# Performance work log

Measured on AMD Instinct MI355X. Metric: run time of the kernel, lower is better.

## Reference

```python
import jax, jax.numpy as jnp
import numpy as np

NUM_RBF = 16
MAX_REL = 32          # max_relative_feature
AUTOREGRESSIVE = True
D_MIN, D_MAX = 2.0, 22.0
LN_EPS = 1e-5


def setup_inputs() -> dict:
    key = jax.random.key(0)
    ks = jax.random.split(key, 6)
    B, L, A, K = 1, 1280, 14, 30
    E_feat, edge_in = 128, 16 + NUM_RBF * 4 * 10  # 656
    X = jax.random.normal(ks[0], (B, L, A, 3), dtype=jnp.float32) * 3.0
    residue_idx = jnp.tile(jnp.arange(L, dtype=jnp.int32)[None], (B, 1))
    chain_labels = jnp.zeros((B, L), dtype=jnp.int32)
    E_idx = jax.random.randint(ks[1], (B, L, K), 0, L, dtype=jnp.int32)
    atom_mask = jnp.ones((B, L, A), dtype=jnp.float32)
    W_pos = jax.random.normal(ks[2], (2 * MAX_REL + 2, 16), dtype=jnp.float32) * 0.1
    b_pos = jnp.zeros((16,), dtype=jnp.float32)
    W_edge = jax.random.normal(ks[3], (edge_in, E_feat), dtype=jnp.float32) * 0.05
    ln_gamma = jnp.ones((E_feat,), dtype=jnp.float32)
    ln_beta = jnp.zeros((E_feat,), dtype=jnp.float32)
    return {"X": X, "residue_idx": residue_idx, "chain_labels": chain_labels,
            "E_idx": E_idx, "atom_mask": atom_mask, "W_pos": W_pos,
            "b_pos": b_pos, "W_edge": W_edge, "ln_gamma": ln_gamma,
            "ln_beta": ln_beta}


def _forward(X, residue_idx, chain_labels, E_idx, W_pos, b_pos, W_edge,
             ln_gamma, ln_beta):
    B, L, A, _ = X.shape
    K = E_idx.shape[-1]
    # backbone atoms in loop order [Ca, N, C, O] -> X indices [1, 0, 2, 3]
    bb = X[:, :, jnp.array([1, 0, 2, 3]), :]          # [B, L, 4, 3]
    sc = X[:, :, 4:, :]                               # [B, L, 10, 3]
    Abb = jnp.transpose(bb, (0, 2, 1, 3))             # [B, 4, L, 3]
    Asc = jnp.transpose(sc, (0, 2, 1, 3))             # [B, 10, L, 3]
    # dense pairwise distances for all 40 (bb, sc) atom pairs: [B,4,10,L,L]
    diff = Abb[:, :, None, :, None, :] - Asc[:, None, :, None, :, :]
    D = jnp.sqrt(jnp.sum(diff * diff, axis=-1) + 1e-6)
    # gather top-k neighbor columns -> [B,4,10,L,K]
    D_nb = jnp.take_along_axis(D, E_idx[:, None, None, :, :], axis=4)
    mu = jnp.linspace(D_MIN, D_MAX, NUM_RBF, dtype=D_nb.dtype)
    sigma = (D_MAX - D_MIN) / NUM_RBF
    RBF = jnp.exp(-(((D_nb[..., None] - mu) / sigma) ** 2))  # [B,4,10,L,K,16]
    if AUTOREGRESSIVE:
        self_edges = (E_idx == jnp.arange(L, dtype=E_idx.dtype)[None, :, None])
        RBF = jnp.where(self_edges[:, None, None, :, :, None], 0.0, RBF)
    # concat order: bb outer, sc inner -> [B,L,K, 4*10*16]
    RBF_all = jnp.transpose(RBF, (0, 3, 4, 1, 2, 5)).reshape(B, L, K, 4 * 10 * NUM_RBF)
    # positional encodings
    offset = residue_idx[:, :, None] - residue_idx[:, None, :]        # [B,L,L]
    offset = jnp.take_along_axis(offset, E_idx, axis=2)               # [B,L,K]
    d_chains = (chain_labels[:, :, None] == chain_labels[:, None, :]).astype(jnp.int32)
    E_chains = jnp.take_along_axis(d_chains, E_idx, axis=2)           # [B,L,K]
    d = jnp.clip(offset + MAX_REL, 0, 2 * MAX_REL) * E_chains + (1 - E_chains) * (2 * MAX_REL + 1)
    d_onehot = jax.nn.one_hot(d, 2 * MAX_REL + 2, dtype=W_pos.dtype)  # [B,L,K,66]
    E_positional = d_onehot @ W_pos + b_pos                           # [B,L,K,16]
    E = jnp.concatenate([E_positional, RBF_all], axis=-1)             # [B,L,K,656]
    E = E @ W_edge                                                    # no bias
    # LayerNorm over last dim
    mean = jnp.mean(E, axis=-1, keepdims=True)
    var = jnp.mean((E - mean) ** 2, axis=-1, keepdims=True)
    E = (E - mean) / jnp.sqrt(var + LN_EPS) * ln_gamma + ln_beta
    return E


def reference(X, residue_idx, chain_labels, E_idx, atom_mask, W_pos, b_pos,
              W_edge, ln_gamma, ln_beta):
    E = _forward(X, residue_idx, chain_labels, E_idx, W_pos, b_pos, W_edge,
                 ln_gamma, ln_beta)
    return (E, E_idx)
```

## Files before the change

kernel.cpp:

```cpp
#include <hip/hip_runtime.h>

typedef short bf16x8 __attribute__((ext_vector_type(8)));
typedef float f32x4  __attribute__((ext_vector_type(4)));

#define L_RES 1280
#define A_ATM 14
#define K_NB  30
#define FEAT  656
#define NKB   21
#define NCH   128
#define FRAG  512
#define E_OUT_OFF (L_RES * K_NB * NCH)
#define NEDGE (L_RES * K_NB)

__device__ __forceinline__ ushort f2bf(float x) {
    union { float f; unsigned u; } v; v.f = x;
    unsigned r = (v.u + 0x7fffu + ((v.u >> 16) & 1u)) >> 16;
    return (ushort)r;
}

__global__ __launch_bounds__(256) void prep_kernel(const float* __restrict__ W,
                                                   ushort* __restrict__ Wpack) {
    int u = blockIdx.x * 256 + threadIdx.x;
    if (u >= 84 * 128) return;
    int kbq = u >> 7, n = u & 127;
    int kb = kbq >> 2, quad = kbq & 3;
    ushort val[8];
#pragma unroll
    for (int j = 0; j < 8; j++) {
        int k = kb * 32 + quad * 8 + j;
        val[j] = (k < FEAT) ? f2bf(W[k * NCH + n]) : (ushort)0;
    }
    ushort* dst = Wpack + (size_t)((((n >> 4) * NKB + kb) * 64 + quad * 16 + (n & 15)) * 8);
    *(ulonglong2*)dst = *(const ulonglong2*)val;
}

__global__ __launch_bounds__(256) void sidechain_fused_kernel(
    const float* __restrict__ X,
    const int*   __restrict__ ridx,
    const int*   __restrict__ clab,
    const int*   __restrict__ Eidx,
    const float* __restrict__ Wpos,
    const float* __restrict__ bpos,
    const ushort* __restrict__ Wpack,
    const float* __restrict__ gamma,
    const float* __restrict__ beta,
    float* __restrict__ out)
{
    __shared__ float scj[4][K_NB][10][3];
    __shared__ float bbs[4][4][3];

    const int t    = threadIdx.x;
    const int w    = t >> 6;
    const int lane = t & 63;
    const int i    = blockIdx.x * 4 + w;
    const int frow = lane & 15;
    const int quad = lane >> 4;

    if (lane < 12) {
        const int perm[4] = {1, 0, 2, 3};
        int a = lane / 3, c = lane - a * 3;
        bbs[w][a][c] = X[(i * A_ATM + perm[a]) * 3 + c];
    }
    for (int idx = lane; idx < K_NB * 30; idx += 64) {
        int e = idx / 30, r = idx - e * 30;
        int a = r / 3, c = r - a * 3;
        int j = Eidx[i * K_NB + e];
        scj[w][e][a][c] = X[(j * A_ATM + 4 + a) * 3 + c];
    }
    if (lane < K_NB) out[E_OUT_OFF + i * K_NB + lane] = (float)Eidx[i * K_NB + lane];

    const int e0 = frow;
    const int e1 = 16 + frow;
    const bool v1 = (e1 < K_NB);
    const int j0 = Eidx[i * K_NB + e0];
    const int j1 = v1 ? Eidx[i * K_NB + e1] : 0;
    const bool rbf0 = (j0 != i);
    const bool rbf1 = v1 && (j1 != i);

    const int ri = ridx[i], ci = clab[i];
    int d0, d1;
    {
        int off0 = ri - ridx[j0] + 32;
        off0 = off0 < 0 ? 0 : (off0 > 64 ? 64 : off0);
        d0 = (ci == clab[j0]) ? off0 : 65;
        int off1 = ri - ridx[j1] + 32;
        off1 = off1 < 0 ? 0 : (off1 > 64 ? 64 : off1);
        d1 = (ci == clab[j1]) ? off1 : 65;
    }

    const ushort* Bbase = Wpack + (size_t)lane * 8;
    f32x4 acc0[8], acc1[8];
#pragma unroll
    for (int n = 0; n < 8; n++) {
        acc0[n] = (f32x4){0.f, 0.f, 0.f, 0.f};
        acc1[n] = (f32x4){0.f, 0.f, 0.f, 0.f};
    }

#pragma unroll
    for (int kb = 0; kb < NKB; kb++) {
        bf16x8 b[8];
#pragma unroll
        for (int n = 0; n < 8; n++)
            b[n] = *(const bf16x8*)(Bbase + (size_t)(n * NKB + kb) * FRAG);

        ushort u0[8], u1[8];
        if (kb == 0 && quad < 2) {
#pragma unroll
            for (int j = 0; j < 8; j++) {
                int c = quad * 8 + j;
                float bp = bpos[c];
                u0[j] = f2bf(Wpos[d0 * 16 + c] + bp);
                u1[j] = v1 ? f2bf(Wpos[d1 * 16 + c] + bp) : (ushort)0;
            }
        } else {
            bool kv = !(kb == NKB - 1 && quad >= 2);
            int p  = kv ? (2 * kb - 1 + (quad >> 1)) : 0;
            int r0 = (quad & 1) * 8;
            int ab = p / 10, as = p - ab * 10;
            float bx = bbs[w][ab][0], by = bbs[w][ab][1], bz = bbs[w][ab][2];
            float x0 = scj[w][e0][as][0], y0 = scj[w][e0][as][1], z0 = scj[w][e0][as][2];
            int e1c = v1 ? e1 : 0;
            float x1 = scj[w][e1c][as][0], y1 = scj[w][e1c][as][1], z1 = scj[w][e1c][as][2];
            float dx0 = bx - x0, dy0 = by - y0, dz0 = bz - z0;
            float dx1 = bx - x1, dy1 = by - y1, dz1 = bz - z1;
            float dist0 = sqrtf(dx0 * dx0 + dy0 * dy0 + dz0 * dz0 + 1e-6f);
            float dist1 = sqrtf(dx1 * dx1 + dy1 * dy1 + dz1 * dz1 + 1e-6f);
            bool m0ok = kv && rbf0, m1ok = kv && rbf1;
#pragma unroll
            for (int j = 0; j < 8; j++) {
                float mu = 2.0f + (float)(r0 + j) * (20.0f / 15.0f);
                float t0 = (dist0 - mu) * 0.8f;
                float t1 = (dist1 - mu) * 0.8f;
                u0[j] = m0ok ? f2bf(__expf(-t0 * t0)) : (ushort)0;
                u1[j] = m1ok ? f2bf(__expf(-t1 * t1)) : (ushort)0;
            }
        }
        bf16x8 a0 = *(const bf16x8*)u0;
        bf16x8 a1 = *(const bf16x8*)u1;
#pragma unroll
        for (int n = 0; n < 8; n++)
            acc0[n] = __builtin_amdgcn_mfma_f32_16x16x32_bf16(a0, b[n], acc0[n], 0, 0, 0);
#pragma unroll
        for (int n = 0; n < 8; n++)
            acc1[n] = __builtin_amdgcn_mfma_f32_16x16x32_bf16(a1, b[n], acc1[n], 0, 0, 0);
    }

    float g[8], bt[8];
#pragma unroll
    for (int n = 0; n < 8; n++) {
        g[n]  = gamma[n * 16 + frow];
        bt[n] = beta[n * 16 + frow];
    }

#pragma unroll
    for (int m = 0; m < 2; m++) {
        f32x4* acc = m ? acc1 : acc0;
#pragma unroll
        for (int r = 0; r < 4; r++) {
            float s = 0.f, q = 0.f;
#pragma unroll
            for (int n = 0; n < 8; n++) {
                float v = acc[n][r];
                s += v; q += v * v;
            }
#pragma unroll
            for (int off = 1; off < 16; off <<= 1) {
                s += __shfl_xor(s, off);
                q += __shfl_xor(q, off);
            }
            float mean = s * (1.0f / 128.0f);
            float var  = q * (1.0f / 128.0f) - mean * mean;
            float rstd = rsqrtf(var + 1e-5f);
            int edge = m * 16 + quad * 4 + r;
            if (edge < K_NB) {
                float* o = out + ((size_t)i * K_NB + edge) * NCH + frow;
#pragma unroll
                for (int n = 0; n < 8; n++)
                    o[n * 16] = (acc[n][r] - mean) * rstd * g[n] + bt[n];
            }
        }
    }
}

extern "C" void kernel_launch(void* const* d_in, const int* in_sizes, int n_in,
                              void* d_out, int out_size, void* d_ws, size_t ws_size,
                              hipStream_t stream) {
    const float* X     = (const float*)d_in[0];
    const int*   ridx  = (const int*)  d_in[1];
    const int*   clab  = (const int*)  d_in[2];
    const int*   Eidx  = (const int*)  d_in[3];
    const float* Wpos  = (const float*)d_in[5];
    const float* bpos  = (const float*)d_in[6];
    const float* Wedge = (const float*)d_in[7];
    const float* gamma = (const float*)d_in[8];
    const float* beta  = (const float*)d_in[9];
    float* out = (float*)d_out;

    ushort* Wpack = (ushort*)d_ws;

    prep_kernel<<<42, 256, 0, stream>>>(Wedge, Wpack);
    sidechain_fused_kernel<<<L_RES / 4, 256, 0, stream>>>(
        X, ridx, clab, Eidx, Wpos, bpos, Wpack, gamma, beta, out);
}
```

Before: 112.5 us.

## Split K dimension across wave pairs with LDS reduction, exp2-based RBF

Each block now handles 2 residues instead of 4. Two waves per residue split the 21 K-blocks of the GEMM and combine their partial accumulators through shared memory before the LayerNorm. This doubles the grid to 640 blocks, which should fill more CUs and halve the serial MFMA chain per wave, at the cost of an extra LDS exchange and a block barrier. The RBF is also rewritten to use exp2 with prescaled constants, and bf16 packing now truncates instead of rounding to nearest even, which slightly changes numerics.

```diff
diff --git a/kernel.cpp b/kernel.cpp
--- a/kernel.cpp
+++ b/kernel.cpp
@@ -1,7 +1,8 @@
 #include <hip/hip_runtime.h>
 
-typedef short bf16x8 __attribute__((ext_vector_type(8)));
-typedef float f32x4  __attribute__((ext_vector_type(4)));
+typedef short    bf16x8 __attribute__((ext_vector_type(8)));
+typedef float    f32x4  __attribute__((ext_vector_type(4)));
+typedef unsigned u32x4  __attribute__((ext_vector_type(4)));
 
 #define L_RES 1280
 #define A_ATM 14
@@ -11,12 +12,15 @@
 #define NCH   128
 #define FRAG  512
 #define E_OUT_OFF (L_RES * K_NB * NCH)
-#define NEDGE (L_RES * K_NB)
 
 __device__ __forceinline__ ushort f2bf(float x) {
     union { float f; unsigned u; } v; v.f = x;
     unsigned r = (v.u + 0x7fffu + ((v.u >> 16) & 1u)) >> 16;
     return (ushort)r;
+}
+__device__ __forceinline__ unsigned pkbf(float lo, float hi) {
+    union { float f; unsigned u; } a, b; a.f = lo; b.f = hi;
+    return (a.u >> 16) | (b.u & 0xffff0000u);
 }
 
 __global__ __launch_bounds__(256) void prep_kernel(const float* __restrict__ W,
@@ -47,49 +51,53 @@
     const float* __restrict__ beta,
     float* __restrict__ out)
 {
-    __shared__ float scj[4][K_NB][10][3];
-    __shared__ float bbs[4][4][3];
-
+    __shared__ __align__(16) float scj[2][K_NB][10][4];
+    __shared__ float bbs[2][4][3];
+    __shared__ __align__(16) float xch[2][16][64][4];
+
+    const int blk  = blockIdx.x;
     const int t    = threadIdx.x;
     const int w    = t >> 6;
     const int lane = t & 63;
-    const int i    = blockIdx.x * 4 + w;
+    const int rh   = w & 1;
+    const int kh   = w >> 1;
+    const int i    = blk * 2 + rh;
     const int frow = lane & 15;
     const int quad = lane >> 4;
 
-    if (lane < 12) {
+    if (t < 24) {
         const int perm[4] = {1, 0, 2, 3};
-        int a = lane / 3, c = lane - a * 3;
-        bbs[w][a][c] = X[(i * A_ATM + perm[a]) * 3 + c];
-    }
-    for (int idx = lane; idx < K_NB * 30; idx += 64) {
-        int e = idx / 30, r = idx - e * 30;
-        int a = r / 3, c = r - a * 3;
-        int j = Eidx[i * K_NB + e];
-        scj[w][e][a][c] = X[(j * A_ATM + 4 + a) * 3 + c];
-    }
-    if (lane < K_NB) out[E_OUT_OFF + i * K_NB + lane] = (float)Eidx[i * K_NB + lane];
-
-    const int e0 = frow;
-    const int e1 = 16 + frow;
+        int r = t / 12, rr = t - r * 12, a = rr / 3, c = rr - a * 3;
+        bbs[r][a][c] = X[((blk * 2 + r) * A_ATM + perm[a]) * 3 + c];
+    }
+#pragma unroll
+    for (int idx = t; idx < 600; idx += 256) {
+        int r = idx / 300, rem = idx - r * 300;
+        int e = rem / 10, a = rem - e * 10;
+        int j = Eidx[(blk * 2 + r) * K_NB + e];
+        const float* xp = X + ((size_t)j * A_ATM + 4 + a) * 3;
+        float4 v = make_float4(xp[0], xp[1], xp[2], 0.f);
+        *(float4*)&scj[r][e][a][0] = v;
+    }
+    __syncthreads();
+
+    const int e0 = frow, e1 = 16 + frow;
     const bool v1 = (e1 < K_NB);
     const int j0 = Eidx[i * K_NB + e0];
     const int j1 = v1 ? Eidx[i * K_NB + e1] : 0;
-    const bool rbf0 = (j0 != i);
-    const bool rbf1 = v1 && (j1 != i);
-
-    const int ri = ridx[i], ci = clab[i];
-    int d0, d1;
+    const bool ok0 = (j0 != i);
+    const bool ok1 = v1 && (j1 != i);
+    int d0 = 65, d1 = 65;
     {
-        int off0 = ri - ridx[j0] + 32;
-        off0 = off0 < 0 ? 0 : (off0 > 64 ? 64 : off0);
-        d0 = (ci == clab[j0]) ? off0 : 65;
-        int off1 = ri - ridx[j1] + 32;
-        off1 = off1 < 0 ? 0 : (off1 > 64 ? 64 : off1);
-        d1 = (ci == clab[j1]) ? off1 : 65;
-    }
-
+        int ci = clab[i], ri = ridx[i];
+        if (ci == clab[j0]) { int o = ri - ridx[j0] + 32; d0 = o < 0 ? 0 : (o > 64 ? 64 : o); }
+        if (ci == clab[j1]) { int o = ri - ridx[j1] + 32; d1 = o < 0 ? 0 : (o > 64 ? 64 : o); }
+    }
+
+    const int kb_lo = kh ? 11 : 0;
+    const int kb_hi = kh ? NKB : 11;
     const ushort* Bbase = Wpack + (size_t)lane * 8;
+
     f32x4 acc0[8], acc1[8];
 #pragma unroll
     for (int n = 0; n < 8; n++) {
@@ -97,87 +105,111 @@
         acc1[n] = (f32x4){0.f, 0.f, 0.f, 0.f};
     }
 
-#pragma unroll
-    for (int kb = 0; kb < NKB; kb++) {
+    const float cs = 0.96089795f;
+    const float mustep = 1.33333333f * cs;
+    const int   r0 = (quad & 1) * 8;
+    const float mubase = (2.0f + (float)r0 * 1.33333333f) * cs;
+
+    for (int kb = kb_lo; kb < kb_hi; kb++) {
         bf16x8 b[8];
 #pragma unroll
         for (int n = 0; n < 8; n++)
             b[n] = *(const bf16x8*)(Bbase + (size_t)(n * NKB + kb) * FRAG);
 
-        ushort u0[8], u1[8];
+        union { u32x4 u; bf16x8 h; } A0, A1;
         if (kb == 0 && quad < 2) {
+            float p0[8], p1[8];
 #pragma unroll
             for (int j = 0; j < 8; j++) {
                 int c = quad * 8 + j;
                 float bp = bpos[c];
-                u0[j] = f2bf(Wpos[d0 * 16 + c] + bp);
-                u1[j] = v1 ? f2bf(Wpos[d1 * 16 + c] + bp) : (ushort)0;
+                p0[j] = Wpos[d0 * 16 + c] + bp;
+                p1[j] = v1 ? (Wpos[d1 * 16 + c] + bp) : 0.f;
+            }
+#pragma unroll
+            for (int jj = 0; jj < 4; jj++) {
+                A0.u[jj] = pkbf(p0[2 * jj], p0[2 * jj + 1]);
+                A1.u[jj] = pkbf(p1[2 * jj], p1[2 * jj + 1]);
             }
         } else {
             bool kv = !(kb == NKB - 1 && quad >= 2);
             int p  = kv ? (2 * kb - 1 + (quad >> 1)) : 0;
-            int r0 = (quad & 1) * 8;
             int ab = p / 10, as = p - ab * 10;
-            float bx = bbs[w][ab][0], by = bbs[w][ab][1], bz = bbs[w][ab][2];
-            float x0 = scj[w][e0][as][0], y0 = scj[w][e0][as][1], z0 = scj[w][e0][as][2];
-            int e1c = v1 ? e1 : 0;
-            float x1 = scj[w][e1c][as][0], y1 = scj[w][e1c][as][1], z1 = scj[w][e1c][as][2];
-            float dx0 = bx - x0, dy0 = by - y0, dz0 = bz - z0;
-            float dx1 = bx - x1, dy1 = by - y1, dz1 = bz - z1;
-            float dist0 = sqrtf(dx0 * dx0 + dy0 * dy0 + dz0 * dz0 + 1e-6f);
-            float dist1 = sqrtf(dx1 * dx1 + dy1 * dy1 + dz1 * dz1 + 1e-6f);
-            bool m0ok = kv && rbf0, m1ok = kv && rbf1;
-#pragma unroll
-            for (int j = 0; j < 8; j++) {
-                float mu = 2.0f + (float)(r0 + j) * (20.0f / 15.0f);
-                float t0 = (dist0 - mu) * 0.8f;
-                float t1 = (dist1 - mu) * 0.8f;
-                u0[j] = m0ok ? f2bf(__expf(-t0 * t0)) : (ushort)0;
-                u1[j] = m1ok ? f2bf(__expf(-t1 * t1)) : (ushort)0;
-            }
-        }
-        bf16x8 a0 = *(const bf16x8*)u0;
-        bf16x8 a1 = *(const bf16x8*)u1;
+            float bx = bbs[rh][ab][0], by = bbs[rh][ab][1], bz = bbs[rh][ab][2];
+            f32x4 s0 = *(const f32x4*)&scj[rh][e0][as][0];
+            f32x4 s1 = *(const f32x4*)&scj[rh][v1 ? e1 : 0][as][0];
+            float dx0 = bx - s0[0], dy0 = by - s0[1], dz0 = bz - s0[2];
+            float dx1 = bx - s1[0], dy1 = by - s1[1], dz1 = bz - s1[2];
+            float dd0 = sqrtf(dx0 * dx0 + dy0 * dy0 + dz0 * dz0 + 1e-6f) * cs - mubase;
+            float dd1 = sqrtf(dx1 * dx1 + dy1 * dy1 + dz1 * dz1 + 1e-6f) * cs - mubase;
+            bool m0 = kv && ok0, m1 = kv && ok1;
+#pragma unroll
+            for (int jj = 0; jj < 4; jj++) {
+                float cA = (float)(2 * jj) * mustep;
+                float cB = (float)(2 * jj + 1) * mustep;
+                float tA0 = dd0 - cA, tB0 = dd0 - cB;
+                float tA1 = dd1 - cA, tB1 = dd1 - cB;
+                unsigned q0 = pkbf(exp2f(-(tA0 * tA0)), exp2f(-(tB0 * tB0)));
+                unsigned q1 = pkbf(exp2f(-(tA1 * tA1)), exp2f(-(tB1 * tB1)));
+                A0.u[jj] = m0 ? q0 : 0u;
+                A1.u[jj] = m1 ? q1 : 0u;
+            }
+        }
 #pragma unroll
         for (int n = 0; n < 8; n++)
-            acc0[n] = __builtin_amdgcn_mfma_f32_16x16x32_bf16(a0, b[n], acc0[n], 0, 0, 0);
+            acc0[n] = __builtin_amdgcn_mfma_f32_16x16x32_bf16(A0.h, b[n], acc0[n], 0, 0, 0);
 #pragma unroll
         for (int n = 0; n < 8; n++)
-            acc1[n] = __builtin_amdgcn_mfma_f32_16x16x32_bf16(a1, b[n], acc1[n], 0, 0, 0);
-    }
-
-    float g[8], bt[8];
-#pragma unroll
-    for (int n = 0; n < 8; n++) {
-        g[n]  = gamma[n * 16 + frow];
-        bt[n] = beta[n * 16 + frow];
-    }
-
-#pragma unroll
-    for (int m = 0; m < 2; m++) {
-        f32x4* acc = m ? acc1 : acc0;
-#pragma unroll
-        for (int r = 0; r < 4; r++) {
-            float s = 0.f, q = 0.f;
-#pragma unroll
-            for (int n = 0; n < 8; n++) {
-                float v = acc[n][r];
-                s += v; q += v * v;
-            }
-#pragma unroll
-            for (int off = 1; off < 16; off <<= 1) {
-                s += __shfl_xor(s, off);
-                q += __shfl_xor(q, off);
-            }
-            float mean = s * (1.0f / 128.0f);
-            float var  = q * (1.0f / 128.0f) - mean * mean;
-            float rstd = rsqrtf(var + 1e-5f);
-            int edge = m * 16 + quad * 4 + r;
-            if (edge < K_NB) {
-                float* o = out + ((size_t)i * K_NB + edge) * NCH + frow;
-#pragma unroll
-                for (int n = 0; n < 8; n++)
-                    o[n * 16] = (acc[n][r] - mean) * rstd * g[n] + bt[n];
+            acc1[n] = __builtin_amdgcn_mfma_f32_16x16x32_bf16(A1.h, b[n], acc1[n], 0, 0, 0);
+    }
+
+    if (kh == 1) {
+#pragma unroll
+        for (int n = 0; n < 8; n++) {
+            *(f32x4*)&xch[rh][n][lane][0]     = acc0[n];
+            *(f32x4*)&xch[rh][8 + n][lane][0] = acc1[n];
+        }
+        if (lane < K_NB) out[E_OUT_OFF + i * K_NB + lane] = (float)Eidx[i * K_NB + lane];
+    }
+    __syncthreads();
+    if (kh == 0) {
+#pragma unroll
+        for (int n = 0; n < 8; n++) {
+            acc0[n] += *(const f32x4*)&xch[rh][n][lane][0];
+            acc1[n] += *(const f32x4*)&xch[rh][8 + n][lane][0];
+        }
+        float g[8], bt[8];
+#pragma unroll
+        for (int n = 0; n < 8; n++) {
+            g[n]  = gamma[n * 16 + frow];
+            bt[n] = beta[n * 16 + frow];
+        }
+#pragma unroll
+        for (int m = 0; m < 2; m++) {
+            f32x4* acc = m ? acc1 : acc0;
+#pragma unroll
+            for (int r = 0; r < 4; r++) {
+                float s = 0.f, q = 0.f;
+#pragma unroll
+                for (int n = 0; n < 8; n++) {
+                    float v = acc[n][r];
+                    s += v; q += v * v;
+                }
+#pragma unroll
+                for (int off = 1; off < 16; off <<= 1) {
+                    s += __shfl_xor(s, off);
+                    q += __shfl_xor(q, off);
+                }
+                float mean = s * (1.0f / 128.0f);
+                float var  = q * (1.0f / 128.0f) - mean * mean;
+                float rstd = rsqrtf(var + 1e-5f);
+                int edge = m * 16 + quad * 4 + r;
+                if (edge < K_NB) {
+                    float* o = out + ((size_t)i * K_NB + edge) * NCH + frow;
+#pragma unroll
+                    for (int n = 0; n < 8; n++)
+                        o[n * 16] = (acc[n][r] - mean) * rstd * g[n] + bt[n];
+                }
             }
         }
     }
@@ -200,6 +232,6 @@
     ushort* Wpack = (ushort*)d_ws;
 
     prep_kernel<<<42, 256, 0, stream>>>(Wedge, Wpack);
-    sidechain_fused_kernel<<<L_RES / 4, 256, 0, stream>>>(
+    sidechain_fused_kernel<<<L_RES / 2, 256, 0, stream>>>(
         X, ridx, clab, Eidx, Wpos, bpos, Wpack, gamma, beta, out);
 }
```

Result: faster. 110.1 us (-2.1%).
